# Kernel optimization log

Hardware: AMD Instinct MI355X
Metric: run time of the kernel (lower is better)

The kernel has to match this reference:

```python
import math
import jax, jax.numpy as jnp
import numpy as np

B, T, D = 2, 1024, 512
H, DK = 8, 64


def setup_inputs() -> dict:
    key = jax.random.key(0)
    ks = jax.random.split(key, 7)
    s = 1.0 / math.sqrt(D)
    x = jax.random.normal(ks[0], (B, T, D), dtype=jnp.float32)
    Wq = jax.random.normal(ks[1], (D, H * DK), dtype=jnp.float32) * s
    Wk = jax.random.normal(ks[2], (D, H * DK), dtype=jnp.float32) * s
    Wv = jax.random.normal(ks[3], (D, H * DK), dtype=jnp.float32) * s
    Wo = jax.random.normal(ks[4], (H * DK, D), dtype=jnp.float32) * s
    Wg = jax.random.normal(ks[5], (D, H * DK), dtype=jnp.float32) * 0.02
    bg = jnp.ones((H * DK,), dtype=jnp.float32)  # gate_bias_init = 1.0
    return {"x": x, "Wq": Wq, "Wk": Wk, "Wv": Wv, "Wo": Wo, "Wg": Wg, "bg": bg}


def reference(x, Wq, Wk, Wv, Wo, Wg, bg):
    b, t, d = x.shape
    Q = jax.nn.relu(x @ Wq).reshape(b, t, H, DK)
    K = jax.nn.relu(x @ Wk).reshape(b, t, H, DK)
    V = (x @ Wv).reshape(b, t, H, DK)
    angle = jnp.arange(t, dtype=x.dtype) * (math.pi / (2 * t))  # (T,)
    cosw = jnp.cos(angle)[None, :, None, None]
    sinw = jnp.sin(angle)[None, :, None, None]
    Qc, Qs = Q * cosw, Q * sinw
    Kc, Ks = K * cosw, K * sinw
    # cumulative KV outer products: (B,T,H,DK,DK)
    Sc = jnp.cumsum(jnp.einsum('bthd,bthe->bthde', Kc, V), axis=1)
    Ss = jnp.cumsum(jnp.einsum('bthd,bthe->bthde', Ks, V), axis=1)
    o = jnp.einsum('bthd,bthde->bthe', Qc, Sc) + jnp.einsum('bthd,bthde->bthe', Qs, Ss)
    zc = jnp.cumsum(Kc, axis=1)
    zs = jnp.cumsum(Ks, axis=1)
    z = jnp.einsum('bthd,bthd->bth', Qc, zc) + jnp.einsum('bthd,bthd->bth', Qs, zs)
    z = jnp.maximum(z, 1e-6)[..., None]
    o = o / z
    gate = jax.nn.sigmoid((x @ Wg + bg).reshape(b, t, H, DK))
    o = o * gate
    return o.reshape(b, t, H * DK) @ Wo
```

## Files before the change

### kernel.cpp

```cpp
#include <hip/hip_runtime.h>
#include <math.h>

#define B_ 2
#define T_ 1024
#define D_ 512
#define H_ 8
#define DK_ 64
#define NBH_ 16
#define C_ 32
#define G_ 32

#define PI_OVER_2T 0.00153398078788564122971808758949f

typedef float f32x4 __attribute__((ext_vector_type(4)));
typedef short s16x8 __attribute__((ext_vector_type(8)));

__device__ __forceinline__ ushort f2bf(float x) {
    unsigned u = __float_as_uint(x);
    unsigned r = (u + 0x7fffu + ((u >> 16) & 1u)) >> 16;
    return (ushort)r;
}
__device__ __forceinline__ float bf2f(ushort u) {
    return __uint_as_float((unsigned)u << 16);
}

__device__ __forceinline__ void async16(void* lds, const void* g) {
    __builtin_amdgcn_global_load_lds(
        (const __attribute__((address_space(1))) void*)g,
        (__attribute__((address_space(3))) void*)lds, 16, 0, 0);
}

__global__ __launch_bounds__(256) void k_conv(
    const float* __restrict__ x,
    const float* __restrict__ Wq, const float* __restrict__ Wk,
    const float* __restrict__ Wv, const float* __restrict__ Wg,
    const float* __restrict__ Wo,
    ushort* __restrict__ xb, ushort* __restrict__ WtAll)
{
    __shared__ float Ts[64][65];
    const int bx = blockIdx.x;
    const int tid = threadIdx.x;
    if (bx < 1024) {
        int i = (bx * 256 + tid) * 4;
        float4 v = *(const float4*)&x[i];
        ushort4 o;
        o.x = f2bf(v.x); o.y = f2bf(v.y); o.z = f2bf(v.z); o.w = f2bf(v.w);
        *(ushort4*)&xb[i] = o;
        return;
    }
    const int bid = bx - 1024;
    const int mi = bid >> 6;
    const int t64 = bid & 63;
    const float* __restrict__ W = (mi == 0) ? Wq : (mi == 1) ? Wk
                                 : (mi == 2) ? Wv : (mi == 3) ? Wg : Wo;
    const int tr = t64 >> 3, tc = t64 & 7;
#pragma unroll
    for (int p = 0; p < 4; p++) {
        int row = p * 16 + (tid >> 4);
        int c4 = (tid & 15) * 4;
        float4 v = *(const float4*)&W[(size_t)(tr * 64 + row) * 512 + tc * 64 + c4];
        Ts[row][c4 + 0] = v.x; Ts[row][c4 + 1] = v.y;
        Ts[row][c4 + 2] = v.z; Ts[row][c4 + 3] = v.w;
    }
    __syncthreads();
    const int nl = tid >> 2, kc = (tid & 3) * 16;
    ushort buf[16];
#pragma unroll
    for (int u = 0; u < 16; u++) buf[u] = f2bf(Ts[kc + u][nl]);
    ushort* dst = WtAll + (size_t)mi * 262144 + (size_t)(tc * 64 + nl) * 512
                  + tr * 64 + kc;
    *(uint4*)dst = *(uint4*)&buf[0];
    *(uint4*)(dst + 8) = *(uint4*)&buf[8];
}

__global__ __launch_bounds__(256) void k_g0(
    const ushort* __restrict__ A, const ushort* __restrict__ WtAll,
    const float* __restrict__ bg,
    ushort* __restrict__ Qg, ushort* __restrict__ Kg,
    ushort* __restrict__ Vg, ushort* __restrict__ Gg,
    ushort* __restrict__ Sst, float* __restrict__ Zst)
{
    __shared__ union {
        struct { ushort As[2][64 * 64]; ushort Bs[2][2 * 64 * 64]; } s;
        struct { ushort KcT[64 * 72]; ushort KsT[64 * 72];
                 ushort VT[64 * 72]; ushort KR[64 * 72];
                 ushort VR[64 * 72]; } e;
    } sm;
    __shared__ float cosR[64], sinR[64];

    const int tid = threadIdx.x;
    const int ct = blockIdx.x;
    const int rowBase = blockIdx.y * 64;
    const bool isKV = (ct >= 8);
    const int matCol = (ct & 7) * 64;
    const ushort* __restrict__ B0 = WtAll + (size_t)(isKV ? 1 : 0) * 262144;
    const ushort* __restrict__ B1 = WtAll + (size_t)(isKV ? 2 : 3) * 262144;

    const int wave = tid >> 6, lane = tid & 63;
    const int q = lane >> 4, ln = lane & 15;
    const int mB = (wave >> 1) * 32, nB = (wave & 1) * 32;

    int fu[2];
    const ushort* gA[2];
    const ushort* gB0[2];
    const ushort* gB1[2];
#pragma unroll
    for (int u = 0; u < 2; u++) {
        int f = tid * 8 + u * 2048;
        int r = f >> 6;
        int gc = ((f >> 3) & 7) ^ (r & 7);
        fu[u] = f;
        gA[u]  = A  + (size_t)(rowBase + r) * 512 + gc * 8;
        gB0[u] = B0 + (size_t)(matCol + r) * 512 + gc * 8;
        gB1[u] = B1 + (size_t)(matCol + r) * 512 + gc * 8;
    }

    f32x4 accA[2][2], accB[2][2];
#pragma unroll
    for (int i = 0; i < 2; i++)
#pragma unroll
        for (int j = 0; j < 2; j++) {
            accA[i][j] = (f32x4){0.f, 0.f, 0.f, 0.f};
            accB[i][j] = (f32x4){0.f, 0.f, 0.f, 0.f};
        }

    int aoff[2][2], boff[2][2];
#pragma unroll
    for (int i = 0; i < 2; i++) {
        int ra = mB + i * 16 + ln;
#pragma unroll
        for (int ks = 0; ks < 2; ks++)
            aoff[i][ks] = ra * 64 + (((ks * 4 + q) ^ (ra & 7)) * 8);
    }
#pragma unroll
    for (int j = 0; j < 2; j++) {
        int rb = nB + j * 16 + ln;
#pragma unroll
        for (int ks = 0; ks < 2; ks++)
            boff[j][ks] = rb * 64 + (((ks * 4 + q) ^ (rb & 7)) * 8);
    }

#pragma unroll
    for (int u = 0; u < 2; u++) {
        async16(&sm.s.As[0][fu[u]], gA[u]);
        async16(&sm.s.Bs[0][fu[u]], gB0[u]);
        async16(&sm.s.Bs[0][4096 + fu[u]], gB1[u]);
    }

    int cur = 0;
    for (int kb = 0; kb < 512; kb += 64) {
        __syncthreads();
        if (kb + 64 < 512) {
            int nxt = cur ^ 1;
#pragma unroll
            for (int u = 0; u < 2; u++) {
                async16(&sm.s.As[nxt][fu[u]], gA[u] + kb + 64);
                async16(&sm.s.Bs[nxt][fu[u]], gB0[u] + kb + 64);
                async16(&sm.s.Bs[nxt][4096 + fu[u]], gB1[u] + kb + 64);
            }
        }
#pragma unroll
        for (int ks = 0; ks < 2; ks++) {
            s16x8 af[2], b0f[2], b1f[2];
#pragma unroll
            for (int i = 0; i < 2; i++)
                af[i] = *(const s16x8*)&sm.s.As[cur][aoff[i][ks]];
#pragma unroll
            for (int j = 0; j < 2; j++) {
                b0f[j] = *(const s16x8*)&sm.s.Bs[cur][boff[j][ks]];
                b1f[j] = *(const s16x8*)&sm.s.Bs[cur][4096 + boff[j][ks]];
            }
#pragma unroll
            for (int i = 0; i < 2; i++)
#pragma unroll
                for (int j = 0; j < 2; j++) {
                    accA[i][j] = __builtin_amdgcn_mfma_f32_16x16x32_bf16(
                        af[i], b0f[j], accA[i][j], 0, 0, 0);
                    accB[i][j] = __builtin_amdgcn_mfma_f32_16x16x32_bf16(
                        af[i], b1f[j], accB[i][j], 0, 0, 0);
                }
        }
        cur ^= 1;
    }
    if (isKV && tid < 64) {
        float a = (float)((rowBase + tid) & 1023) * PI_OVER_2T;
        cosR[tid] = cosf(a);
        sinR[tid] = sinf(a);
    }
    __syncthreads();

    if (!isKV) {
        ushort* QT = sm.e.KcT;
        ushort* GT = sm.e.KsT;
#pragma unroll
        for (int i = 0; i < 2; i++)
#pragma unroll
            for (int j = 0; j < 2; j++) {
                int colL = nB + j * 16 + ln;
                float bgv = bg[matCol + colL];
#pragma unroll
                for (int r = 0; r < 4; r++) {
                    int rowL = mB + i * 16 + q * 4 + r;
                    QT[rowL * 72 + colL] = f2bf(fmaxf(accA[i][j][r], 0.f));
                    GT[rowL * 72 + colL] =
                        f2bf(1.f / (1.f + expf(-(accB[i][j][r] + bgv))));
                }
            }
        __syncthreads();
#pragma unroll
        for (int it = 0; it < 2; it++) {
            int row = it * 32 + (tid >> 3), sub = tid & 7;
            uint4 qv = *(const uint4*)&QT[row * 72 + sub * 8];
            uint4 gv = *(const uint4*)&GT[row * 72 + sub * 8];
            size_t go = (size_t)(rowBase + row) * 512 + matCol + sub * 8;
            *(uint4*)&Qg[go] = qv;
            *(uint4*)&Gg[go] = gv;
        }
        return;
    }

    const int h = ct - 8;
    const int b = rowBase >> 10;
    const int c = wave >> 1;
    const int gG = ((rowBase & 1023) >> 5) + c;
    const int blk = (b * 8 + h) * 32 + gG;

    float zc[2] = {0.f, 0.f}, zs[2] = {0.f, 0.f};
#pragma unroll
    for (int i = 0; i < 2; i++)
#pragma unroll
        for (int r = 0; r < 4; r++) {
            int tLoc = mB + i * 16 + q * 4 + r;
            float ca = cosR[tLoc], sa = sinR[tLoc];
#pragma unroll
            for (int j = 0; j < 2; j++) {
                int col = nB + j * 16 + ln;
                float kv = fmaxf(accA[i][j][r], 0.f);
                float vv = accB[i][j][r];
                sm.e.KR[tLoc * 72 + col] = f2bf(kv);
                sm.e.VR[tLoc * 72 + col] = f2bf(vv);
                float kc = kv * ca, ks = kv * sa;
                sm.e.KcT[col * 72 + tLoc] = f2bf(kc);
                sm.e.KsT[col * 72 + tLoc] = f2bf(ks);
                sm.e.VT [col * 72 + tLoc] = f2bf(vv);
                zc[j] += kc; zs[j] += ks;
            }
        }
#pragma unroll
    for (int j = 0; j < 2; j++) {
        zc[j] += __shfl_xor(zc[j], 16); zc[j] += __shfl_xor(zc[j], 32);
        zs[j] += __shfl_xor(zs[j], 16); zs[j] += __shfl_xor(zs[j], 32);
    }
    if (q == 0) {
#pragma unroll
        for (int j = 0; j < 2; j++) {
            int d = nB + j * 16 + ln;
            Zst[(size_t)blk * 128 + d] = zc[j];
            Zst[(size_t)blk * 128 + 64 + d] = zs[j];
        }
    }
    __syncthreads();

#pragma unroll
    for (int it = 0; it < 2; it++) {
        int row = it * 32 + (tid >> 3), sub = tid & 7;
        uint4 kv4 = *(const uint4*)&sm.e.KR[row * 72 + sub * 8];
        uint4 vv4 = *(const uint4*)&sm.e.VR[row * 72 + sub * 8];
        size_t go = (size_t)(rowBase + row) * 512 + h * 64 + sub * 8;
        *(uint4*)&Kg[go] = kv4;
        *(uint4*)&Vg[go] = vv4;
    }

    {
        const int eh = (wave & 1) * 32;
        ushort* Sp = Sst + (size_t)blk * 8192;
        s16x8 av[2];
#pragma unroll
        for (int fi = 0; fi < 2; fi++)
            av[fi] = *(const s16x8*)&sm.e.VT[(eh + fi * 16 + ln) * 72
                                            + c * 32 + q * 8];
#pragma unroll
        for (int fj = 0; fj < 4; fj++) {
            s16x8 bc = *(const s16x8*)&sm.e.KcT[(fj * 16 + ln) * 72
                                                + c * 32 + q * 8];
            s16x8 bs = *(const s16x8*)&sm.e.KsT[(fj * 16 + ln) * 72
                                                + c * 32 + q * 8];
#pragma unroll
            for (int fi = 0; fi < 2; fi++) {
                f32x4 sc = __builtin_amdgcn_mfma_f32_16x16x32_bf16(
                    av[fi], bc, (f32x4){0.f, 0.f, 0.f, 0.f}, 0, 0, 0);
                f32x4 ss = __builtin_amdgcn_mfma_f32_16x16x32_bf16(
                    av[fi], bs, (f32x4){0.f, 0.f, 0.f, 0.f}, 0, 0, 0);
#pragma unroll
                for (int rr = 0; rr < 4; rr++) {
                    int e = eh + fi * 16 + q * 4 + rr;
                    int d = fj * 16 + ln;
                    Sp[e * 64 + d] = f2bf(sc[rr]);
                    Sp[4096 + e * 64 + d] = f2bf(ss[rr]);
                }
            }
        }
    }
}

template<int MODE, int TM, int TN, int BK>
__global__ __launch_bounds__(256) void k_gemm(
    const ushort* __restrict__ A, const ushort* __restrict__ Bt,
    const float* __restrict__ bg,
    void* __restrict__ O0v, void* __restrict__ O1v,
    void* __restrict__ O2v, void* __restrict__ O3v)
{
    constexpr int WM = TM / 2, WN = TN / 2;
    constexpr int FM = WM / 16, FN = WN / 16;
    constexpr int CH = BK / 8;
    constexpr int SH = (BK == 32) ? 1 : 0;
    constexpr int KS = BK / 32;
    constexpr int NA = TM * BK / 2048;
    constexpr int NB = TN * BK / 2048;
    static_assert(TM == 64 && TN == 32, "epilogue specialized");

    __shared__ ushort As[2][TM * BK];
    __shared__ ushort Bs[2][TN * BK];

    const int tid = threadIdx.x;
    const int ct = blockIdx.x;
    const int rowBase = blockIdx.y * TM;

    const int matCol = ct * TN;
    const ushort* __restrict__ Bmat = Bt;

    const int wave = tid >> 6, lane = tid & 63;
    const int q = lane >> 4, ln = lane & 15;
    const int mB = (wave >> 1) * WM, nB = (wave & 1) * WN;

    int fuA[NA], fuB[NB];
    const ushort* gA[NA];
    const ushort* gB[NB];
#pragma unroll
    for (int u = 0; u < NA; u++) {
        int fu = tid * 8 + u * 2048;
        int r = fu / BK;
        int slot = (fu >> 3) & (CH - 1);
        int gc = slot ^ ((r >> SH) & (CH - 1));
        fuA[u] = fu;
        gA[u] = A + (size_t)(rowBase + r) * 512 + gc * 8;
    }
#pragma unroll
    for (int u = 0; u < NB; u++) {
        int fu = tid * 8 + u * 2048;
        int r = fu / BK;
        int slot = (fu >> 3) & (CH - 1);
        int gc = slot ^ ((r >> SH) & (CH - 1));
        fuB[u] = fu;
        gB[u] = Bmat + (size_t)(matCol + r) * 512 + gc * 8;
    }

    f32x4 acc[FM][FN];
#pragma unroll
    for (int i = 0; i < FM; i++)
#pragma unroll
        for (int j = 0; j < FN; j++) acc[i][j] = (f32x4){0.f, 0.f, 0.f, 0.f};

    int aoff[FM][KS], boff[FN][KS];
#pragma unroll
    for (int i = 0; i < FM; i++) {
        int ra = mB + i * 16 + ln;
#pragma unroll
        for (int ks = 0; ks < KS; ks++)
            aoff[i][ks] = ra * BK + (((ks * 4 + q) ^ ((ra >> SH) & (CH - 1))) * 8);
    }
#pragma unroll
    for (int j = 0; j < FN; j++) {
        int rb = nB + j * 16 + ln;
#pragma unroll
        for (int ks = 0; ks < KS; ks++)
            boff[j][ks] = rb * BK + (((ks * 4 + q) ^ ((rb >> SH) & (CH - 1))) * 8);
    }

#pragma unroll
    for (int u = 0; u < NA; u++) async16(&As[0][fuA[u]], gA[u]);
#pragma unroll
    for (int u = 0; u < NB; u++) async16(&Bs[0][fuB[u]], gB[u]);

    int cur = 0;
    for (int kb = 0; kb < 512; kb += BK) {
        __syncthreads();
        if (kb + BK < 512) {
#pragma unroll
            for (int u = 0; u < NA; u++)
                async16(&As[cur ^ 1][fuA[u]], gA[u] + kb + BK);
#pragma unroll
            for (int u = 0; u < NB; u++)
                async16(&Bs[cur ^ 1][fuB[u]], gB[u] + kb + BK);
        }
#pragma unroll
        for (int ks = 0; ks < KS; ks++) {
            s16x8 af[FM], bf[FN];
#pragma unroll
            for (int i = 0; i < FM; i++)
                af[i] = *(const s16x8*)&As[cur][aoff[i][ks]];
#pragma unroll
            for (int j = 0; j < FN; j++)
                bf[j] = *(const s16x8*)&Bs[cur][boff[j][ks]];
#pragma unroll
            for (int i = 0; i < FM; i++)
#pragma unroll
                for (int j = 0; j < FN; j++)
                    acc[i][j] = __builtin_amdgcn_mfma_f32_16x16x32_bf16(
                        af[i], bf[j], acc[i][j], 0, 0, 0);
        }
        cur ^= 1;
    }
    __syncthreads();

    float* Ot = (float*)&As[0][0];
#pragma unroll
    for (int i = 0; i < FM; i++)
#pragma unroll
        for (int j = 0; j < FN; j++) {
            int colL = nB + j * 16 + ln;
#pragma unroll
            for (int r = 0; r < 4; r++) {
                int rowL = mB + i * 16 + q * 4 + r;
                Ot[rowL * 36 + colL] = acc[i][j][r];
            }
        }
    __syncthreads();

    float* __restrict__ Out = (float*)O0v;
    {
        int row = tid >> 2, sub = tid & 3;
        float4 a0 = *(const float4*)&Ot[row * 36 + sub * 8];
        float4 a1 = *(const float4*)&Ot[row * 36 + sub * 8 + 4];
        size_t go = (size_t)(rowBase + row) * 512 + matCol + sub * 8;
        *(float4*)&Out[go] = a0;
        *(float4*)&Out[go + 4] = a1;
    }
}

__global__ __launch_bounds__(256) void k_scan(
    ushort* __restrict__ Sst, float* __restrict__ Zst)
{
    int id = blockIdx.x * 256 + threadIdx.x;
    if (id < 32768) {
        int bh = id >> 11, i4 = (id & 2047) * 4;
        size_t base = (size_t)bh * (G_ * 8192) + i4;
        ushort4 v[G_];
#pragma unroll
        for (int g = 0; g < G_; g++)
            v[g] = *(const ushort4*)&Sst[base + (size_t)g * 8192];
        float rx = 0.f, ry = 0.f, rz = 0.f, rw = 0.f;
#pragma unroll
        for (int g = 0; g < G_; g++) {
            ushort4 t = v[g];
            ushort4 o;
            o.x = f2bf(rx); o.y = f2bf(ry); o.z = f2bf(rz); o.w = f2bf(rw);
            *(ushort4*)&Sst[base + (size_t)g * 8192] = o;
            rx += bf2f(t.x); ry += bf2f(t.y);
            rz += bf2f(t.z); rw += bf2f(t.w);
        }
    } else {
        int id2 = id - 32768;
        if (id2 >= 512) return;
        int bh = id2 >> 5, i4 = (id2 & 31) * 4;
        size_t base = (size_t)bh * (G_ * 128) + i4;
        float4 v[G_];
#pragma unroll
        for (int g = 0; g < G_; g++)
            v[g] = *(const float4*)&Zst[base + (size_t)g * 128];
        float4 run = make_float4(0.f, 0.f, 0.f, 0.f);
#pragma unroll
        for (int g = 0; g < G_; g++) {
            float4 t = v[g];
            *(float4*)&Zst[base + (size_t)g * 128] = run;
            run.x += t.x; run.y += t.y; run.z += t.z; run.w += t.w;
        }
    }
}

__global__ __launch_bounds__(256) void k_out_chunk(
    const ushort* __restrict__ Qg, const ushort* __restrict__ Kg,
    const ushort* __restrict__ Vg, const ushort* __restrict__ Gg,
    const ushort* __restrict__ Sst, const float* __restrict__ Zst,
    ushort* __restrict__ Op)
{
    __shared__ ushort VT[64 * 40];
    __shared__ ushort Pb[32 * 40];
    __shared__ float zinv[32];
    __shared__ float Ot[32 * 68];

    const int blk = blockIdx.x;
    const int bh = blk >> 5, g = blk & 31;
    const int b = bh >> 3, h = bh & 7;
    const int tid = threadIdx.x;
    const int rBase = b * T_ + g * C_;
    const int colB = h * DK_;
    const int wave = tid >> 6, lane = tid & 63;
    const int q = lane >> 4, ln = lane & 15;

    {
        int row = tid >> 3, c8 = (tid & 7) * 8;
        uint4 vraw = *(const uint4*)&Vg[(size_t)(rBase + row) * D_ + colB + c8];
        const ushort* vp = (const ushort*)&vraw;
#pragma unroll
        for (int u = 0; u < 8; u++) VT[(c8 + u) * 40 + row] = vp[u];
    }

    const int mi = wave >> 1, njp = wave & 1;
    const ushort* qrow = Qg + (size_t)(rBase + mi * 16 + ln) * D_ + colB;
    s16x8 aq0 = *(const s16x8*)&qrow[q * 8];
    s16x8 aq1 = *(const s16x8*)&qrow[32 + q * 8];
    {
        const ushort* krow = Kg + (size_t)(rBase + njp * 16 + ln) * D_ + colB;
        s16x8 bk0 = *(const s16x8*)&krow[q * 8];
        s16x8 bk1 = *(const s16x8*)&krow[32 + q * 8];
        f32x4 pacc = __builtin_amdgcn_mfma_f32_16x16x32_bf16(
            aq0, bk0, (f32x4){0.f, 0.f, 0.f, 0.f}, 0, 0, 0);
        pacc = __builtin_amdgcn_mfma_f32_16x16x32_bf16(aq1, bk1, pacc, 0, 0, 0);
        int sl = njp * 16 + ln;
#pragma unroll
        for (int r = 0; r < 4; r++) {
            int tl = mi * 16 + q * 4 + r;
            float w = (sl <= tl) ? cosf((float)(tl - sl) * PI_OVER_2T) : 0.f;
            Pb[tl * 40 + sl] = f2bf(pacc[r] * w);
        }
    }
    __syncthreads();

    {
        int t = tid >> 3, sub = tid & 7;
        uint4 qraw = *(const uint4*)&Qg[(size_t)(rBase + t) * D_ + colB + sub * 8];
        const ushort* qp = (const ushort*)&qraw;
        const float* zcp = Zst + (size_t)blk * 128 + sub * 8;
        float4 zc0 = *(const float4*)&zcp[0];
        float4 zc1 = *(const float4*)&zcp[4];
        float4 zs0 = *(const float4*)&zcp[64];
        float4 zs1 = *(const float4*)&zcp[68];
        float pc = 0.f, ps = 0.f;
        float zcv[8] = {zc0.x, zc0.y, zc0.z, zc0.w, zc1.x, zc1.y, zc1.z, zc1.w};
        float zsv[8] = {zs0.x, zs0.y, zs0.z, zs0.w, zs1.x, zs1.y, zs1.z, zs1.w};
#pragma unroll
        for (int u = 0; u < 8; u++) {
            float qf = bf2f(qp[u]);
            pc += qf * zcv[u]; ps += qf * zsv[u];
        }
        float pr = 0.f;
#pragma unroll
        for (int u = 0; u < 4; u++) pr += bf2f(Pb[t * 40 + sub * 4 + u]);
#pragma unroll
        for (int m = 1; m < 8; m <<= 1) {
            pc += __shfl_xor(pc, m);
            ps += __shfl_xor(ps, m);
            pr += __shfl_xor(pr, m);
        }
        if (sub == 0) {
            float at = (float)(g * C_ + t) * PI_OVER_2T;
            float z = cosf(at) * pc + sinf(at) * ps + pr;
            zinv[t] = 1.f / fmaxf(z, 1e-6f);
        }
    }
    __syncthreads();

    {
        float cr[4], sr[4];
#pragma unroll
        for (int r = 0; r < 4; r++) {
            int tl = mi * 16 + q * 4 + r;
            float at = (float)(g * C_ + tl) * PI_OVER_2T;
            cr[r] = cosf(at); sr[r] = sinf(at);
        }
        s16x8 pf = *(const s16x8*)&Pb[(mi * 16 + ln) * 40 + q * 8];
        const ushort* Sp = Sst + (size_t)blk * 8192;
#pragma unroll
        for (int jj = 0; jj < 2; jj++) {
            int nj = 2 * (wave & 1) + jj;
            const ushort* scp = Sp + (nj * 16 + ln) * 64;
            s16x8 bc0 = *(const s16x8*)&scp[q * 8];
            s16x8 bc1 = *(const s16x8*)&scp[32 + q * 8];
            s16x8 bs0 = *(const s16x8*)&scp[4096 + q * 8];
            s16x8 bs1 = *(const s16x8*)&scp[4096 + 32 + q * 8];
            s16x8 bv  = *(const s16x8*)&VT[(nj * 16 + ln) * 40 + q * 8];
            f32x4 accP = __builtin_amdgcn_mfma_f32_16x16x32_bf16(
                pf, bv, (f32x4){0.f, 0.f, 0.f, 0.f}, 0, 0, 0);
            f32x4 accC = __builtin_amdgcn_mfma_f32_16x16x32_bf16(
                aq0, bc0, (f32x4){0.f, 0.f, 0.f, 0.f}, 0, 0, 0);
            accC = __builtin_amdgcn_mfma_f32_16x16x32_bf16(aq1, bc1, accC, 0, 0, 0);
            f32x4 accS = __builtin_amdgcn_mfma_f32_16x16x32_bf16(
                aq0, bs0, (f32x4){0.f, 0.f, 0.f, 0.f}, 0, 0, 0);
            accS = __builtin_amdgcn_mfma_f32_16x16x32_bf16(aq1, bs1, accS, 0, 0, 0);
#pragma unroll
            for (int r = 0; r < 4; r++) {
                int tl = mi * 16 + q * 4 + r;
                Ot[tl * 68 + nj * 16 + ln] =
                    (accP[r] + cr[r] * accC[r] + sr[r] * accS[r]) * zinv[tl];
            }
        }
    }
    __syncthreads();

    {
        int t = tid >> 3, sub = tid & 7;
        size_t go = (size_t)(rBase + t) * D_ + colB + sub * 8;
        uint4 graw = *(const uint4*)&Gg[go];
        const ushort* gp = (const ushort*)&graw;
        const float* op = &Ot[t * 68 + sub * 8];
        ushort buf[8];
#pragma unroll
        for (int u = 0; u < 8; u++)
            buf[u] = f2bf(op[u] * bf2f(gp[u]));
        *(uint4*)&Op[go] = *(uint4*)&buf[0];
    }
}

extern "C" void kernel_launch(void* const* d_in, const int* in_sizes, int n_in,
                              void* d_out, int out_size, void* d_ws, size_t ws_size,
                              hipStream_t stream)
{
    const float* x  = (const float*)d_in[0];
    const float* Wq = (const float*)d_in[1];
    const float* Wk = (const float*)d_in[2];
    const float* Wv = (const float*)d_in[3];
    const float* Wo = (const float*)d_in[4];
    const float* Wg = (const float*)d_in[5];
    const float* bg = (const float*)d_in[6];
    float* out = (float*)d_out;

    ushort* wsu = (ushort*)d_ws;
    ushort* xb    = wsu;
    ushort* WtAll = xb + 1048576;
    ushort* Qg    = WtAll + 1310720;
    ushort* Kg    = Qg + 1048576;
    ushort* Vg    = Kg + 1048576;
    ushort* Gg    = Vg + 1048576;
    ushort* Sst   = Gg + 1048576;
    ushort* Opb   = Sst + 4194304;
    float*  Zst   = (float*)(Opb + 1048576);

    dim3 blk(256);
    k_conv<<<dim3(1344), blk, 0, stream>>>(x, Wq, Wk, Wv, Wg, Wo, xb, WtAll);
    k_g0<<<dim3(16, 32), blk, 0, stream>>>(
        xb, WtAll, bg, Qg, Kg, Vg, Gg, Sst, Zst);
    k_scan<<<dim3(130), blk, 0, stream>>>(Sst, Zst);
    k_out_chunk<<<dim3(NBH_ * G_), blk, 0, stream>>>(
        Qg, Kg, Vg, Gg, Sst, Zst, Opb);
    k_gemm<1, 64, 32, 64><<<dim3(16, 32), blk, 0, stream>>>(
        Opb, WtAll + (size_t)4 * 262144, nullptr,
        out, nullptr, nullptr, nullptr);
}
```

Before: 104.7 us.

## Halve GEMM row tiles and parallelize chunk-state scan across more threads

```diff
diff --git a/kernel.cpp b/kernel.cpp
--- a/kernel.cpp
+++ b/kernel.cpp
@@ -73,7 +73,7 @@
     *(uint4*)(dst + 8) = *(uint4*)&buf[8];
 }
 
-__global__ __launch_bounds__(256) void k_g0(
+__global__ __launch_bounds__(256) void k_g0b(
     const ushort* __restrict__ A, const ushort* __restrict__ WtAll,
     const float* __restrict__ bg,
     ushort* __restrict__ Qg, ushort* __restrict__ Kg,
@@ -81,16 +81,16 @@
     ushort* __restrict__ Sst, float* __restrict__ Zst)
 {
     __shared__ union {
-        struct { ushort As[2][64 * 64]; ushort Bs[2][2 * 64 * 64]; } s;
-        struct { ushort KcT[64 * 72]; ushort KsT[64 * 72];
-                 ushort VT[64 * 72]; ushort KR[64 * 72];
-                 ushort VR[64 * 72]; } e;
+        struct { ushort As[2][2048]; ushort Bs[2][8192]; } s;
+        struct { ushort KcT[64 * 40]; ushort KsT[64 * 40];
+                 ushort VT[64 * 40];
+                 ushort KR[32 * 72]; ushort VR[32 * 72]; } e;
     } sm;
-    __shared__ float cosR[64], sinR[64];
+    __shared__ float cosR[32], sinR[32];
 
     const int tid = threadIdx.x;
     const int ct = blockIdx.x;
-    const int rowBase = blockIdx.y * 64;
+    const int rowBase = blockIdx.y * 32;
     const bool isKV = (ct >= 8);
     const int matCol = (ct & 7) * 64;
     const ushort* __restrict__ B0 = WtAll + (size_t)(isKV ? 1 : 0) * 262144;
@@ -98,10 +98,18 @@
 
     const int wave = tid >> 6, lane = tid & 63;
     const int q = lane >> 4, ln = lane & 15;
-    const int mB = (wave >> 1) * 32, nB = (wave & 1) * 32;
-
-    int fu[2];
-    const ushort* gA[2];
+    const int nB = wave * 16;
+
+    int fA;
+    const ushort* gA;
+    {
+        int f = tid * 8;
+        int r = f >> 6;
+        int gc = ((f >> 3) & 7) ^ (r & 7);
+        fA = f;
+        gA = A + (size_t)(rowBase + r) * 512 + gc * 8;
+    }
+    int fB[2];
     const ushort* gB0[2];
     const ushort* gB1[2];
 #pragma unroll
@@ -109,42 +117,38 @@
         int f = tid * 8 + u * 2048;
         int r = f >> 6;
         int gc = ((f >> 3) & 7) ^ (r & 7);
-        fu[u] = f;
-        gA[u]  = A  + (size_t)(rowBase + r) * 512 + gc * 8;
+        fB[u] = f;
         gB0[u] = B0 + (size_t)(matCol + r) * 512 + gc * 8;
         gB1[u] = B1 + (size_t)(matCol + r) * 512 + gc * 8;
     }
 
-    f32x4 accA[2][2], accB[2][2];
-#pragma unroll
-    for (int i = 0; i < 2; i++)
-#pragma unroll
-        for (int j = 0; j < 2; j++) {
-            accA[i][j] = (f32x4){0.f, 0.f, 0.f, 0.f};
-            accB[i][j] = (f32x4){0.f, 0.f, 0.f, 0.f};
-        }
-
-    int aoff[2][2], boff[2][2];
+    f32x4 accA[2], accB[2];
 #pragma unroll
     for (int i = 0; i < 2; i++) {
-        int ra = mB + i * 16 + ln;
+        accA[i] = (f32x4){0.f, 0.f, 0.f, 0.f};
+        accB[i] = (f32x4){0.f, 0.f, 0.f, 0.f};
+    }
+
+    int aoff[2][2], boff[2];
+#pragma unroll
+    for (int i = 0; i < 2; i++) {
+        int ra = i * 16 + ln;
 #pragma unroll
         for (int ks = 0; ks < 2; ks++)
             aoff[i][ks] = ra * 64 + (((ks * 4 + q) ^ (ra & 7)) * 8);
     }
-#pragma unroll
-    for (int j = 0; j < 2; j++) {
-        int rb = nB + j * 16 + ln;
+    {
+        int rb = nB + ln;
 #pragma unroll
         for (int ks = 0; ks < 2; ks++)
-            boff[j][ks] = rb * 64 + (((ks * 4 + q) ^ (rb & 7)) * 8);
-    }
-
+            boff[ks] = rb * 64 + (((ks * 4 + q) ^ (rb & 7)) * 8);
+    }
+
+    async16(&sm.s.As[0][fA], gA);
 #pragma unroll
     for (int u = 0; u < 2; u++) {
-        async16(&sm.s.As[0][fu[u]], gA[u]);
-        async16(&sm.s.Bs[0][fu[u]], gB0[u]);
-        async16(&sm.s.Bs[0][4096 + fu[u]], gB1[u]);
+        async16(&sm.s.Bs[0][fB[u]], gB0[u]);
+        async16(&sm.s.Bs[0][4096 + fB[u]], gB1[u]);
     }
 
     int cur = 0;
@@ -152,37 +156,32 @@
         __syncthreads();
         if (kb + 64 < 512) {
             int nxt = cur ^ 1;
+            async16(&sm.s.As[nxt][fA], gA + kb + 64);
 #pragma unroll
             for (int u = 0; u < 2; u++) {
-                async16(&sm.s.As[nxt][fu[u]], gA[u] + kb + 64);
-                async16(&sm.s.Bs[nxt][fu[u]], gB0[u] + kb + 64);
-                async16(&sm.s.Bs[nxt][4096 + fu[u]], gB1[u] + kb + 64);
+                async16(&sm.s.Bs[nxt][fB[u]], gB0[u] + kb + 64);
+                async16(&sm.s.Bs[nxt][4096 + fB[u]], gB1[u] + kb + 64);
             }
         }
 #pragma unroll
         for (int ks = 0; ks < 2; ks++) {
-            s16x8 af[2], b0f[2], b1f[2];
+            s16x8 af[2];
 #pragma unroll
             for (int i = 0; i < 2; i++)
                 af[i] = *(const s16x8*)&sm.s.As[cur][aoff[i][ks]];
-#pragma unroll
-            for (int j = 0; j < 2; j++) {
-                b0f[j] = *(const s16x8*)&sm.s.Bs[cur][boff[j][ks]];
-                b1f[j] = *(const s16x8*)&sm.s.Bs[cur][4096 + boff[j][ks]];
+            s16x8 b0f = *(const s16x8*)&sm.s.Bs[cur][boff[ks]];
+            s16x8 b1f = *(const s16x8*)&sm.s.Bs[cur][4096 + boff[ks]];
+#pragma unroll
+            for (int i = 0; i < 2; i++) {
+                accA[i] = __builtin_amdgcn_mfma_f32_16x16x32_bf16(
+                    af[i], b0f, accA[i], 0, 0, 0);
+                accB[i] = __builtin_amdgcn_mfma_f32_16x16x32_bf16(
+                    af[i], b1f, accB[i], 0, 0, 0);
             }
-#pragma unroll
-            for (int i = 0; i < 2; i++)
-#pragma unroll
-                for (int j = 0; j < 2; j++) {
-                    accA[i][j] = __builtin_amdgcn_mfma_f32_16x16x32_bf16(
-                        af[i], b0f[j], accA[i][j], 0, 0, 0);
-                    accB[i][j] = __builtin_amdgcn_mfma_f32_16x16x32_bf16(
-                        af[i], b1f[j], accB[i][j], 0, 0, 0);
-                }
         }
         cur ^= 1;
     }
-    if (isKV && tid < 64) {
+    if (isKV && tid < 32) {
         float a = (float)((rowBase + tid) & 1023) * PI_OVER_2T;
         cosR[tid] = cosf(a);
         sinR[tid] = sinf(a);
@@ -192,24 +191,20 @@
     if (!isKV) {
         ushort* QT = sm.e.KcT;
         ushort* GT = sm.e.KsT;
+        const int colL = nB + ln;
+        const float bgv = bg[matCol + colL];
 #pragma unroll
         for (int i = 0; i < 2; i++)
 #pragma unroll
-            for (int j = 0; j < 2; j++) {
-                int colL = nB + j * 16 + ln;
-                float bgv = bg[matCol + colL];
-#pragma unroll
-                for (int r = 0; r < 4; r++) {
-                    int rowL = mB + i * 16 + q * 4 + r;
-                    QT[rowL * 72 + colL] = f2bf(fmaxf(accA[i][j][r], 0.f));
-                    GT[rowL * 72 + colL] =
-                        f2bf(1.f / (1.f + expf(-(accB[i][j][r] + bgv))));
-                }
+            for (int r = 0; r < 4; r++) {
+                int rowL = i * 16 + q * 4 + r;
+                QT[rowL * 72 + colL] = f2bf(fmaxf(accA[i][r], 0.f));
+                GT[rowL * 72 + colL] =
+                    f2bf(1.f / (1.f + expf(-(accB[i][r] + bgv))));
             }
         __syncthreads();
-#pragma unroll
-        for (int it = 0; it < 2; it++) {
-            int row = it * 32 + (tid >> 3), sub = tid & 7;
+        {
+            int row = tid >> 3, sub = tid & 7;
             uint4 qv = *(const uint4*)&QT[row * 72 + sub * 8];
             uint4 gv = *(const uint4*)&GT[row * 72 + sub * 8];
             size_t go = (size_t)(rowBase + row) * 512 + matCol + sub * 8;
@@ -221,49 +216,37 @@
 
     const int h = ct - 8;
     const int b = rowBase >> 10;
-    const int c = wave >> 1;
-    const int gG = ((rowBase & 1023) >> 5) + c;
+    const int gG = (rowBase & 1023) >> 5;
     const int blk = (b * 8 + h) * 32 + gG;
-
-    float zc[2] = {0.f, 0.f}, zs[2] = {0.f, 0.f};
+    const int col = nB + ln;
+
+    float zc = 0.f, zs = 0.f;
 #pragma unroll
     for (int i = 0; i < 2; i++)
 #pragma unroll
         for (int r = 0; r < 4; r++) {
-            int tLoc = mB + i * 16 + q * 4 + r;
+            int tLoc = i * 16 + q * 4 + r;
             float ca = cosR[tLoc], sa = sinR[tLoc];
-#pragma unroll
-            for (int j = 0; j < 2; j++) {
-                int col = nB + j * 16 + ln;
-                float kv = fmaxf(accA[i][j][r], 0.f);
-                float vv = accB[i][j][r];
-                sm.e.KR[tLoc * 72 + col] = f2bf(kv);
-                sm.e.VR[tLoc * 72 + col] = f2bf(vv);
-                float kc = kv * ca, ks = kv * sa;
-                sm.e.KcT[col * 72 + tLoc] = f2bf(kc);
-                sm.e.KsT[col * 72 + tLoc] = f2bf(ks);
-                sm.e.VT [col * 72 + tLoc] = f2bf(vv);
-                zc[j] += kc; zs[j] += ks;
-            }
-        }
-#pragma unroll
-    for (int j = 0; j < 2; j++) {
-        zc[j] += __shfl_xor(zc[j], 16); zc[j] += __shfl_xor(zc[j], 32);
-        zs[j] += __shfl_xor(zs[j], 16); zs[j] += __shfl_xor(zs[j], 32);
-    }
+            float kv = fmaxf(accA[i][r], 0.f);
+            float vv = accB[i][r];
+            sm.e.KR[tLoc * 72 + col] = f2bf(kv);
+            sm.e.VR[tLoc * 72 + col] = f2bf(vv);
+            float kc = kv * ca, ks_ = kv * sa;
+            sm.e.KcT[col * 40 + tLoc] = f2bf(kc);
+            sm.e.KsT[col * 40 + tLoc] = f2bf(ks_);
+            sm.e.VT [col * 40 + tLoc] = f2bf(vv);
+            zc += kc; zs += ks_;
+        }
+    zc += __shfl_xor(zc, 16); zc += __shfl_xor(zc, 32);
+    zs += __shfl_xor(zs, 16); zs += __shfl_xor(zs, 32);
     if (q == 0) {
-#pragma unroll
-        for (int j = 0; j < 2; j++) {
-            int d = nB + j * 16 + ln;
-            Zst[(size_t)blk * 128 + d] = zc[j];
-            Zst[(size_t)blk * 128 + 64 + d] = zs[j];
-        }
-    }
-    __syncthreads();
-
-#pragma unroll
-    for (int it = 0; it < 2; it++) {
-        int row = it * 32 + (tid >> 3), sub = tid & 7;
+        Zst[(size_t)blk * 128 + col] = zc;
+        Zst[(size_t)blk * 128 + 64 + col] = zs;
+    }
+    __syncthreads();
+
+    {
+        int row = tid >> 3, sub = tid & 7;
         uint4 kv4 = *(const uint4*)&sm.e.KR[row * 72 + sub * 8];
         uint4 vv4 = *(const uint4*)&sm.e.VR[row * 72 + sub * 8];
         size_t go = (size_t)(rowBase + row) * 512 + h * 64 + sub * 8;
@@ -272,207 +255,92 @@
     }
 
     {
-        const int eh = (wave & 1) * 32;
         ushort* Sp = Sst + (size_t)blk * 8192;
-        s16x8 av[2];
-#pragma unroll
-        for (int fi = 0; fi < 2; fi++)
-            av[fi] = *(const s16x8*)&sm.e.VT[(eh + fi * 16 + ln) * 72
-                                            + c * 32 + q * 8];
+        s16x8 av = *(const s16x8*)&sm.e.VT[(wave * 16 + ln) * 40 + q * 8];
 #pragma unroll
         for (int fj = 0; fj < 4; fj++) {
-            s16x8 bc = *(const s16x8*)&sm.e.KcT[(fj * 16 + ln) * 72
-                                                + c * 32 + q * 8];
-            s16x8 bs = *(const s16x8*)&sm.e.KsT[(fj * 16 + ln) * 72
-                                                + c * 32 + q * 8];
-#pragma unroll
-            for (int fi = 0; fi < 2; fi++) {
-                f32x4 sc = __builtin_amdgcn_mfma_f32_16x16x32_bf16(
-                    av[fi], bc, (f32x4){0.f, 0.f, 0.f, 0.f}, 0, 0, 0);
-                f32x4 ss = __builtin_amdgcn_mfma_f32_16x16x32_bf16(
-                    av[fi], bs, (f32x4){0.f, 0.f, 0.f, 0.f}, 0, 0, 0);
-#pragma unroll
-                for (int rr = 0; rr < 4; rr++) {
-                    int e = eh + fi * 16 + q * 4 + rr;
-                    int d = fj * 16 + ln;
-                    Sp[e * 64 + d] = f2bf(sc[rr]);
-                    Sp[4096 + e * 64 + d] = f2bf(ss[rr]);
-                }
+            s16x8 bc = *(const s16x8*)&sm.e.KcT[(fj * 16 + ln) * 40 + q * 8];
+            s16x8 bs = *(const s16x8*)&sm.e.KsT[(fj * 16 + ln) * 40 + q * 8];
+            f32x4 sc = __builtin_amdgcn_mfma_f32_16x16x32_bf16(
+                av, bc, (f32x4){0.f, 0.f, 0.f, 0.f}, 0, 0, 0);
+            f32x4 ss = __builtin_amdgcn_mfma_f32_16x16x32_bf16(
+                av, bs, (f32x4){0.f, 0.f, 0.f, 0.f}, 0, 0, 0);
+#pragma unroll
+            for (int rr = 0; rr < 4; rr++) {
+                int e = wave * 16 + q * 4 + rr;
+                int d = fj * 16 + ln;
+                Sp[e * 64 + d] = f2bf(sc[rr]);
+                Sp[4096 + e * 64 + d] = f2bf(ss[rr]);
             }
         }
     }
 }
 
-template<int MODE, int TM, int TN, int BK>
-__global__ __launch_bounds__(256) void k_gemm(
-    const ushort* __restrict__ A, const ushort* __restrict__ Bt,
-    const float* __restrict__ bg,
-    void* __restrict__ O0v, void* __restrict__ O1v,
-    void* __restrict__ O2v, void* __restrict__ O3v)
-{
-    constexpr int WM = TM / 2, WN = TN / 2;
-    constexpr int FM = WM / 16, FN = WN / 16;
-    constexpr int CH = BK / 8;
-    constexpr int SH = (BK == 32) ? 1 : 0;
-    constexpr int KS = BK / 32;
-    constexpr int NA = TM * BK / 2048;
-    constexpr int NB = TN * BK / 2048;
-    static_assert(TM == 64 && TN == 32, "epilogue specialized");
-
-    __shared__ ushort As[2][TM * BK];
-    __shared__ ushort Bs[2][TN * BK];
-
-    const int tid = threadIdx.x;
-    const int ct = blockIdx.x;
-    const int rowBase = blockIdx.y * TM;
-
-    const int matCol = ct * TN;
-    const ushort* __restrict__ Bmat = Bt;
-
-    const int wave = tid >> 6, lane = tid & 63;
-    const int q = lane >> 4, ln = lane & 15;
-    const int mB = (wave >> 1) * WM, nB = (wave & 1) * WN;
-
-    int fuA[NA], fuB[NB];
-    const ushort* gA[NA];
-    const ushort* gB[NB];
-#pragma unroll
-    for (int u = 0; u < NA; u++) {
-        int fu = tid * 8 + u * 2048;
-        int r = fu / BK;
-        int slot = (fu >> 3) & (CH - 1);
-        int gc = slot ^ ((r >> SH) & (CH - 1));
-        fuA[u] = fu;
-        gA[u] = A + (size_t)(rowBase + r) * 512 + gc * 8;
-    }
-#pragma unroll
-    for (int u = 0; u < NB; u++) {
-        int fu = tid * 8 + u * 2048;
-        int r = fu / BK;
-        int slot = (fu >> 3) & (CH - 1);
-        int gc = slot ^ ((r >> SH) & (CH - 1));
-        fuB[u] = fu;
-        gB[u] = Bmat + (size_t)(matCol + r) * 512 + gc * 8;
-    }
-
-    f32x4 acc[FM][FN];
-#pragma unroll
-    for (int i = 0; i < FM; i++)
-#pragma unroll
-        for (int j = 0; j < FN; j++) acc[i][j] = (f32x4){0.f, 0.f, 0.f, 0.f};
-
-    int aoff[FM][KS], boff[FN][KS];
-#pragma unroll
-    for (int i = 0; i < FM; i++) {
-        int ra = mB + i * 16 + ln;
-#pragma unroll
-        for (int ks = 0; ks < KS; ks++)
-            aoff[i][ks] = ra * BK + (((ks * 4 + q) ^ ((ra >> SH) & (CH - 1))) * 8);
-    }
-#pragma unroll
-    for (int j = 0; j < FN; j++) {
-        int rb = nB + j * 16 + ln;
-#pragma unroll
-        for (int ks = 0; ks < KS; ks++)
-            boff[j][ks] = rb * BK + (((ks * 4 + q) ^ ((rb >> SH) & (CH - 1))) * 8);
-    }
-
-#pragma unroll
-    for (int u = 0; u < NA; u++) async16(&As[0][fuA[u]], gA[u]);
-#pragma unroll
-    for (int u = 0; u < NB; u++) async16(&Bs[0][fuB[u]], gB[u]);
-
-    int cur = 0;
-    for (int kb = 0; kb < 512; kb += BK) {
-        __syncthreads();
-        if (kb + BK < 512) {
-#pragma unroll
-            for (int u = 0; u < NA; u++)
-                async16(&As[cur ^ 1][fuA[u]], gA[u] + kb + BK);
-#pragma unroll
-            for (int u = 0; u < NB; u++)
-                async16(&Bs[cur ^ 1][fuB[u]], gB[u] + kb + BK);
-        }
-#pragma unroll
-        for (int ks = 0; ks < KS; ks++) {
-            s16x8 af[FM], bf[FN];
-#pragma unroll
-            for (int i = 0; i < FM; i++)
-                af[i] = *(const s16x8*)&As[cur][aoff[i][ks]];
-#pragma unroll
-            for (int j = 0; j < FN; j++)
-                bf[j] = *(const s16x8*)&Bs[cur][boff[j][ks]];
-#pragma unroll
-            for (int i = 0; i < FM; i++)
-#pragma unroll
-                for (int j = 0; j < FN; j++)
-                    acc[i][j] = __builtin_amdgcn_mfma_f32_16x16x32_bf16(
-                        af[i], bf[j], acc[i][j], 0, 0, 0);
-        }
-        cur ^= 1;
-    }
-    __syncthreads();
-
-    float* Ot = (float*)&As[0][0];
-#pragma unroll
-    for (int i = 0; i < FM; i++)
-#pragma unroll
-        for (int j = 0; j < FN; j++) {
-            int colL = nB + j * 16 + ln;
-#pragma unroll
-            for (int r = 0; r < 4; r++) {
-                int rowL = mB + i * 16 + q * 4 + r;
-                Ot[rowL * 36 + colL] = acc[i][j][r];
-            }
-        }
-    __syncthreads();
-
-    float* __restrict__ Out = (float*)O0v;
-    {
-        int row = tid >> 2, sub = tid & 3;
-        float4 a0 = *(const float4*)&Ot[row * 36 + sub * 8];
-        float4 a1 = *(const float4*)&Ot[row * 36 + sub * 8 + 4];
-        size_t go = (size_t)(rowBase + row) * 512 + matCol + sub * 8;
-        *(float4*)&Out[go] = a0;
-        *(float4*)&Out[go + 4] = a1;
-    }
-}
-
-__global__ __launch_bounds__(256) void k_scan(
+__global__ __launch_bounds__(256) void k_scan2(
     ushort* __restrict__ Sst, float* __restrict__ Zst)
 {
     int id = blockIdx.x * 256 + threadIdx.x;
-    if (id < 32768) {
-        int bh = id >> 11, i4 = (id & 2047) * 4;
-        size_t base = (size_t)bh * (G_ * 8192) + i4;
-        ushort4 v[G_];
-#pragma unroll
-        for (int g = 0; g < G_; g++)
-            v[g] = *(const ushort4*)&Sst[base + (size_t)g * 8192];
-        float rx = 0.f, ry = 0.f, rz = 0.f, rw = 0.f;
-#pragma unroll
-        for (int g = 0; g < G_; g++) {
-            ushort4 t = v[g];
+    if (id < 131072) {
+        int chain = id >> 2, s = id & 3;
+        int bh = chain >> 11, i4 = (chain & 2047) * 4;
+        size_t base = (size_t)bh * (G_ * 8192) + i4 + (size_t)(s * 8) * 8192;
+        ushort4 v[8];
+#pragma unroll
+        for (int k = 0; k < 8; k++)
+            v[k] = *(const ushort4*)&Sst[base + (size_t)k * 8192];
+        float sx = 0.f, sy = 0.f, sz = 0.f, sw = 0.f;
+#pragma unroll
+        for (int k = 0; k < 8; k++) {
+            sx += bf2f(v[k].x); sy += bf2f(v[k].y);
+            sz += bf2f(v[k].z); sw += bf2f(v[k].w);
+        }
+        float px = 0.f, py = 0.f, pz = 0.f, pw = 0.f;
+#pragma unroll
+        for (int d = 1; d < 4; d++) {
+            float tx = __shfl_up(sx, d, 4);
+            float ty = __shfl_up(sy, d, 4);
+            float tz = __shfl_up(sz, d, 4);
+            float tw = __shfl_up(sw, d, 4);
+            if (s >= d) { px += tx; py += ty; pz += tz; pw += tw; }
+        }
+        float rx = px, ry = py, rz = pz, rw = pw;
+#pragma unroll
+        for (int k = 0; k < 8; k++) {
+            ushort4 t = v[k];
             ushort4 o;
             o.x = f2bf(rx); o.y = f2bf(ry); o.z = f2bf(rz); o.w = f2bf(rw);
-            *(ushort4*)&Sst[base + (size_t)g * 8192] = o;
+            *(ushort4*)&Sst[base + (size_t)k * 8192] = o;
             rx += bf2f(t.x); ry += bf2f(t.y);
             rz += bf2f(t.z); rw += bf2f(t.w);
         }
-    } else {
-        int id2 = id - 32768;
-        if (id2 >= 512) return;
-        int bh = id2 >> 5, i4 = (id2 & 31) * 4;
-        size_t base = (size_t)bh * (G_ * 128) + i4;
-        float4 v[G_];
-#pragma unroll
-        for (int g = 0; g < G_; g++)
-            v[g] = *(const float4*)&Zst[base + (size_t)g * 128];
-        float4 run = make_float4(0.f, 0.f, 0.f, 0.f);
-#pragma unroll
-        for (int g = 0; g < G_; g++) {
-            float4 t = v[g];
-            *(float4*)&Zst[base + (size_t)g * 128] = run;
+    } else if (id < 133120) {
+        int u = id - 131072;
+        int chain = u >> 2, s = u & 3;
+        int bh = chain >> 5, i4 = (chain & 31) * 4;
+        size_t base = (size_t)bh * (G_ * 128) + i4 + (size_t)(s * 8) * 128;
+        float4 v[8];
+#pragma unroll
+        for (int k = 0; k < 8; k++)
+            v[k] = *(const float4*)&Zst[base + (size_t)k * 128];
+        float4 sg = make_float4(0.f, 0.f, 0.f, 0.f);
+#pragma unroll
+        for (int k = 0; k < 8; k++) {
+            sg.x += v[k].x; sg.y += v[k].y; sg.z += v[k].z; sg.w += v[k].w;
+        }
+        float4 p = make_float4(0.f, 0.f, 0.f, 0.f);
+#pragma unroll
+        for (int d = 1; d < 4; d++) {
+            float tx = __shfl_up(sg.x, d, 4);
+            float ty = __shfl_up(sg.y, d, 4);
+            float tz = __shfl_up(sg.z, d, 4);
+            float tw = __shfl_up(sg.w, d, 4);
+            if (s >= d) { p.x += tx; p.y += ty; p.z += tz; p.w += tw; }
+        }
+        float4 run = p;
+#pragma unroll
+        for (int k = 0; k < 8; k++) {
+            float4 t = v[k];
+            *(float4*)&Zst[base + (size_t)k * 128] = run;
             run.x += t.x; run.y += t.y; run.z += t.z; run.w += t.w;
         }
     }
@@ -612,6 +480,78 @@
     }
 }
 
+__global__ __launch_bounds__(256) void k_gemm2(
+    const ushort* __restrict__ A, const ushort* __restrict__ Bt,
+    float* __restrict__ Out)
+{
+    __shared__ ushort As[2][2048];
+    __shared__ ushort Bs[2][2048];
+
+    const int tid = threadIdx.x;
+    const int matCol = blockIdx.x * 32;
+    const int rowBase = blockIdx.y * 32;
+    const int wave = tid >> 6, lane = tid & 63;
+    const int q = lane >> 4, ln = lane & 15;
+    const int mB = (wave >> 1) * 16, nB = (wave & 1) * 16;
+
+    int fA;
+    const ushort* gA;
+    const ushort* gB;
+    {
+        int f = tid * 8;
+        int r = f >> 6;
+        int gc = ((f >> 3) & 7) ^ (r & 7);
+        fA = f;
+        gA = A  + (size_t)(rowBase + r) * 512 + gc * 8;
+        gB = Bt + (size_t)(matCol + r) * 512 + gc * 8;
+    }
+
+    f32x4 acc = (f32x4){0.f, 0.f, 0.f, 0.f};
+    int aoff[2], boff[2];
+    {
+        int ra = mB + ln;
+        int rb = nB + ln;
+#pragma unroll
+        for (int ks = 0; ks < 2; ks++) {
+            aoff[ks] = ra * 64 + (((ks * 4 + q) ^ (ra & 7)) * 8);
+            boff[ks] = rb * 64 + (((ks * 4 + q) ^ (rb & 7)) * 8);
+        }
+    }
+
+    async16(&As[0][fA], gA);
+    async16(&Bs[0][fA], gB);
+
+    int cur = 0;
+    for (int kb = 0; kb < 512; kb += 64) {
+        __syncthreads();
+        if (kb + 64 < 512) {
+            async16(&As[cur ^ 1][fA], gA + kb + 64);
+            async16(&Bs[cur ^ 1][fA], gB + kb + 64);
+        }
+#pragma unroll
+        for (int ks = 0; ks < 2; ks++) {
+            s16x8 af = *(const s16x8*)&As[cur][aoff[ks]];
+            s16x8 bf = *(const s16x8*)&Bs[cur][boff[ks]];
+            acc = __builtin_amdgcn_mfma_f32_16x16x32_bf16(af, bf, acc, 0, 0, 0);
+        }
+        cur ^= 1;
+    }
+    __syncthreads();
+
+    float* Ot = (float*)&As[0][0];
+#pragma unroll
+    for (int r = 0; r < 4; r++)
+        Ot[(mB + q * 4 + r) * 36 + nB + ln] = acc[r];
+    __syncthreads();
+
+    {
+        int row = tid >> 3, sub = tid & 7;
+        float4 a0 = *(const float4*)&Ot[row * 36 + sub * 4];
+        size_t go = (size_t)(rowBase + row) * 512 + matCol + sub * 4;
+        *(float4*)&Out[go] = a0;
+    }
+}
+
 extern "C" void kernel_launch(void* const* d_in, const int* in_sizes, int n_in,
                               void* d_out, int out_size, void* d_ws, size_t ws_size,
                               hipStream_t stream)
@@ -638,12 +578,11 @@
 
     dim3 blk(256);
     k_conv<<<dim3(1344), blk, 0, stream>>>(x, Wq, Wk, Wv, Wg, Wo, xb, WtAll);
-    k_g0<<<dim3(16, 32), blk, 0, stream>>>(
+    k_g0b<<<dim3(16, 64), blk, 0, stream>>>(
         xb, WtAll, bg, Qg, Kg, Vg, Gg, Sst, Zst);
-    k_scan<<<dim3(130), blk, 0, stream>>>(Sst, Zst);
+    k_scan2<<<dim3(520), blk, 0, stream>>>(Sst, Zst);
     k_out_chunk<<<dim3(NBH_ * G_), blk, 0, stream>>>(
         Qg, Kg, Vg, Gg, Sst, Zst, Opb);
-    k_gemm<1, 64, 32, 64><<<dim3(16, 32), blk, 0, stream>>>(
-        Opb, WtAll + (size_t)4 * 262144, nullptr,
-        out, nullptr, nullptr, nullptr);
-}
+    k_gemm2<<<dim3(16, 64), blk, 0, stream>>>(
+        Opb, WtAll + (size_t)4 * 262144, out);
+}
```

Result: slower. 109.7 us (+4.8%).
